# Kernel tuning notes

Hardware: AMD Instinct MI355X
Metric: run time of the kernel (lower is better)

Reference implementation:

```python
import jax, jax.numpy as jnp
import numpy as np

D_MODEL = 1024
HEADS = 16
D_K = D_MODEL // HEADS


def setup_inputs() -> dict:
    key = jax.random.key(0)
    k1, k2, k3, k4, k5 = jax.random.split(key, 5)
    B, S = 4, 2048
    q = jax.random.normal(k1, (B, S, D_MODEL), dtype=jnp.float32)
    # causal mask, broadcastable to [B, H, S, S]; 0 => masked
    mask = jnp.tril(jnp.ones((S, S), dtype=jnp.int32))[None, None, :, :]
    scale = 1.0 / np.sqrt(D_MODEL)
    w_q = jax.random.normal(k2, (D_MODEL, D_MODEL), dtype=jnp.float32) * scale
    w_k = jax.random.normal(k3, (D_MODEL, D_MODEL), dtype=jnp.float32) * scale
    w_v = jax.random.normal(k4, (D_MODEL, D_MODEL), dtype=jnp.float32) * scale
    w_o = jax.random.normal(k5, (D_MODEL, D_MODEL), dtype=jnp.float32) * scale
    return {"q": q, "mask": mask, "w_q": w_q, "w_k": w_k, "w_v": w_v, "w_o": w_o}


def reference(q, mask, w_q, w_k, w_v, w_o):
    B, S, _ = q.shape
    # Linear(bias=False): x @ W^T, then split heads -> [B, H, S, d_k]
    def proj(x, w):
        return (x @ w.T).reshape(B, S, HEADS, D_K).transpose(0, 2, 1, 3)

    Q = proj(q, w_q)
    K = proj(q, w_k)
    V = proj(q, w_v)
    scores = jnp.einsum("bhsd,bhtd->bhst", Q, K) / np.sqrt(D_K)
    scores = jnp.where(mask == 0, jnp.float32(-1e9), scores)
    attn = jax.nn.softmax(scores, axis=-1)  # dropout p=0.0 -> identity
    out = jnp.einsum("bhst,bhtd->bhsd", attn, V)
    out = out.transpose(0, 2, 1, 3).reshape(B, S, D_MODEL)
    return out @ w_o.T
```

## Files before the change

kernel.cpp:

```cpp
#include <hip/hip_runtime.h>
#include <math.h>

#define BATCH 4
#define S_LEN 2048
#define DM    1024
#define NH    16
#define DK    64

typedef __attribute__((ext_vector_type(8))) short short8;
typedef __attribute__((ext_vector_type(4))) float f32x4;

static __device__ __forceinline__ unsigned short bf_hi(float x) {
    union { float f; unsigned u; } c; c.f = x;
    return (unsigned short)(c.u >> 16);
}
static __device__ __forceinline__ float bf_f(unsigned short h) {
    union { unsigned u; float f; } c; c.u = ((unsigned)h) << 16;
    return c.f;
}
static __device__ __forceinline__ unsigned short bf_rnd(float x) {
    union { float f; unsigned u; } c; c.f = x;
    unsigned r = c.u + 0x7fffu + ((c.u >> 16) & 1u);
    return (unsigned short)(r >> 16);
}

__global__ __launch_bounds__(256, 2)
void gemm_bf16x3(const float* __restrict__ X, const float* __restrict__ W,
                 float* __restrict__ C, int M, int N, int K)
{
    __shared__ unsigned short Xh[128][40], Xl[128][40];
    __shared__ unsigned short Wh[128][40], Wl[128][40];

    const int tid  = threadIdx.x;
    const int lane = tid & 63;
    const int wid  = tid >> 6;
    const int lrow = lane & 15;
    const int lgrp = lane >> 4;
    const int bm = blockIdx.y * 128;
    const int bn = blockIdx.x * 128;
    const int wm = (wid & 1) * 64;
    const int wn = (wid >> 1) * 64;

    const f32x4 fzero = {0.f, 0.f, 0.f, 0.f};
    f32x4 acc[4][4];
#pragma unroll
    for (int i = 0; i < 4; ++i)
#pragma unroll
        for (int j = 0; j < 4; ++j) acc[i][j] = fzero;

    const int srow = tid >> 2;
    const int sc8  = (tid & 3) * 8;

    for (int kt = 0; kt < K; kt += 32) {
#pragma unroll
        for (int i = 0; i < 2; ++i) {
            const int row = srow + i * 64;
            const float* xp = X + (size_t)(bm + row) * K + kt + sc8;
            const float* wp = W + (size_t)(bn + row) * K + kt + sc8;
            float4 a0 = *(const float4*)xp, a1 = *(const float4*)(xp + 4);
            float4 b0 = *(const float4*)wp, b1 = *(const float4*)(wp + 4);
            float va[8] = {a0.x,a0.y,a0.z,a0.w,a1.x,a1.y,a1.z,a1.w};
            float vb[8] = {b0.x,b0.y,b0.z,b0.w,b1.x,b1.y,b1.z,b1.w};
            short8 xh, xl, wh, wl;
#pragma unroll
            for (int j = 0; j < 8; ++j) {
                unsigned short h = bf_hi(va[j]);
                xh[j] = (short)h; xl[j] = (short)bf_hi(va[j] - bf_f(h));
                unsigned short g = bf_hi(vb[j]);
                wh[j] = (short)g; wl[j] = (short)bf_hi(vb[j] - bf_f(g));
            }
            *(short8*)&Xh[row][sc8] = xh; *(short8*)&Xl[row][sc8] = xl;
            *(short8*)&Wh[row][sc8] = wh; *(short8*)&Wl[row][sc8] = wl;
        }
        __syncthreads();

        short8 ah[4], al[4], bh[4], bl[4];
#pragma unroll
        for (int t = 0; t < 4; ++t) {
            ah[t] = *(const short8*)&Xh[wm + t*16 + lrow][lgrp*8];
            al[t] = *(const short8*)&Xl[wm + t*16 + lrow][lgrp*8];
            bh[t] = *(const short8*)&Wh[wn + t*16 + lrow][lgrp*8];
            bl[t] = *(const short8*)&Wl[wn + t*16 + lrow][lgrp*8];
        }
#pragma unroll
        for (int mt = 0; mt < 4; ++mt)
#pragma unroll
            for (int nt = 0; nt < 4; ++nt) {
                acc[mt][nt] = __builtin_amdgcn_mfma_f32_16x16x32_bf16(ah[mt], bh[nt], acc[mt][nt], 0, 0, 0);
                acc[mt][nt] = __builtin_amdgcn_mfma_f32_16x16x32_bf16(ah[mt], bl[nt], acc[mt][nt], 0, 0, 0);
                acc[mt][nt] = __builtin_amdgcn_mfma_f32_16x16x32_bf16(al[mt], bh[nt], acc[mt][nt], 0, 0, 0);
            }
        __syncthreads();
    }

#pragma unroll
    for (int mt = 0; mt < 4; ++mt)
#pragma unroll
        for (int nt = 0; nt < 4; ++nt)
#pragma unroll
            for (int r = 0; r < 4; ++r)
                C[(size_t)(bm + wm + mt*16 + lgrp*4 + r) * N + bn + wn + nt*16 + lrow]
                    = acc[mt][nt][r];
}

__global__ __launch_bounds__(256, 2)
void attn_mfma(const float* __restrict__ Qg, const float* __restrict__ Kg,
               const float* __restrict__ Vg, float* __restrict__ Og)
{
    __shared__ unsigned short Ksh[64][72], Ksl[64][72];
    __shared__ unsigned short Vth[64][72], Vtl[64][72];
    __shared__ unsigned short Ps[4][16][72];

    const int tid  = threadIdx.x;
    const int lane = tid & 63;
    const int wid  = tid >> 6;
    const int lrow = lane & 15;
    const int lgrp = lane >> 4;

    const int rt = (int)(gridDim.x - 1u - blockIdx.x);
    const int bh = blockIdx.y;
    const int b  = bh >> 4;
    const int h  = bh & 15;

    const size_t base = (size_t)b * S_LEN * DM + (size_t)h * DK;
    const int row0 = rt * 64;

    short8 qh[2], ql[2];
#pragma unroll
    for (int c = 0; c < 2; ++c) {
        const float* qp = Qg + base + (size_t)(row0 + wid*16 + lrow) * DM + c*32 + lgrp*8;
        float4 a0 = *(const float4*)qp, a1 = *(const float4*)(qp + 4);
        float v[8] = {a0.x,a0.y,a0.z,a0.w,a1.x,a1.y,a1.z,a1.w};
#pragma unroll
        for (int j = 0; j < 8; ++j) {
            float x = v[j] * 0.125f;
            unsigned short hh = bf_hi(x);
            qh[c][j] = (short)hh;
            ql[c][j] = (short)bf_hi(x - bf_f(hh));
        }
    }

    const f32x4 fzero = {0.f, 0.f, 0.f, 0.f};
    f32x4 o[4];
    float m[4], l[4];
#pragma unroll
    for (int i = 0; i < 4; ++i) { o[i] = fzero; m[i] = -1e30f; l[i] = 0.f; }

    const int kkey = tid >> 3;
    const int kc8  = (tid & 7) * 8;
    const int vk0  = (tid >> 4) * 4;
    const int vd0  = (tid & 15) * 4;

    for (int kt = 0; kt <= rt; ++kt) {
        const float* Kb = Kg + base + (size_t)(kt * 64) * DM;
        const float* Vb = Vg + base + (size_t)(kt * 64) * DM;

#pragma unroll
        for (int i = 0; i < 2; ++i) {
            const int key = kkey + i * 32;
            const float* kp = Kb + (size_t)key * DM + kc8;
            float4 a0 = *(const float4*)kp, a1 = *(const float4*)(kp + 4);
            float v[8] = {a0.x,a0.y,a0.z,a0.w,a1.x,a1.y,a1.z,a1.w};
            short8 hh, ll;
#pragma unroll
            for (int j = 0; j < 8; ++j) {
                unsigned short t = bf_hi(v[j]);
                hh[j] = (short)t; ll[j] = (short)bf_hi(v[j] - bf_f(t));
            }
            *(short8*)&Ksh[key][kc8] = hh;
            *(short8*)&Ksl[key][kc8] = ll;
        }
        {
            float4 vv[4];
#pragma unroll
            for (int kk = 0; kk < 4; ++kk)
                vv[kk] = *(const float4*)(Vb + (size_t)(vk0 + kk) * DM + vd0);
#pragma unroll
            for (int j = 0; j < 4; ++j) {
                unsigned short h4[4], g4[4];
#pragma unroll
                for (int kk = 0; kk < 4; ++kk) {
                    float x = ((const float*)&vv[kk])[j];
                    h4[kk] = bf_hi(x);
                    g4[kk] = bf_hi(x - bf_f(h4[kk]));
                }
                uint2 wh, wl;
                wh.x = (unsigned)h4[0] | ((unsigned)h4[1] << 16);
                wh.y = (unsigned)h4[2] | ((unsigned)h4[3] << 16);
                wl.x = (unsigned)g4[0] | ((unsigned)g4[1] << 16);
                wl.y = (unsigned)g4[2] | ((unsigned)g4[3] << 16);
                *(uint2*)&Vth[vd0 + j][vk0] = wh;
                *(uint2*)&Vtl[vd0 + j][vk0] = wl;
            }
        }
        __syncthreads();

        f32x4 s[4];
#pragma unroll
        for (int t = 0; t < 4; ++t) s[t] = fzero;
#pragma unroll
        for (int t = 0; t < 4; ++t)
#pragma unroll
            for (int c = 0; c < 2; ++c) {
                short8 kh = *(const short8*)&Ksh[t*16 + lrow][c*32 + lgrp*8];
                short8 kl = *(const short8*)&Ksl[t*16 + lrow][c*32 + lgrp*8];
                s[t] = __builtin_amdgcn_mfma_f32_16x16x32_bf16(qh[c], kh, s[t], 0, 0, 0);
                s[t] = __builtin_amdgcn_mfma_f32_16x16x32_bf16(ql[c], kh, s[t], 0, 0, 0);
                s[t] = __builtin_amdgcn_mfma_f32_16x16x32_bf16(qh[c], kl, s[t], 0, 0, 0);
            }

        if (kt == rt) {
            const int qloc = wid * 16 + lgrp * 4;
#pragma unroll
            for (int t = 0; t < 4; ++t)
#pragma unroll
                for (int r = 0; r < 4; ++r)
                    if (t*16 + lrow > qloc + r) s[t][r] = -1e30f;
        }

        float pm[4];
#pragma unroll
        for (int r = 0; r < 4; ++r)
            pm[r] = fmaxf(fmaxf(s[0][r], s[1][r]), fmaxf(s[2][r], s[3][r]));
#pragma unroll
        for (int off = 8; off >= 1; off >>= 1)
#pragma unroll
            for (int r = 0; r < 4; ++r)
                pm[r] = fmaxf(pm[r], __shfl_xor(pm[r], off));

        float rs[4], rowsum[4];
#pragma unroll
        for (int r = 0; r < 4; ++r) {
            float mn = fmaxf(m[r], pm[r]);
            rs[r] = __expf(m[r] - mn);
            m[r] = mn;
            rowsum[r] = 0.f;
        }
#pragma unroll
        for (int t = 0; t < 4; ++t)
#pragma unroll
            for (int r = 0; r < 4; ++r) {
                float p = __expf(s[t][r] - m[r]);
                s[t][r] = p;
                rowsum[r] += p;
            }
#pragma unroll
        for (int off = 8; off >= 1; off >>= 1)
#pragma unroll
            for (int r = 0; r < 4; ++r)
                rowsum[r] += __shfl_xor(rowsum[r], off);
#pragma unroll
        for (int r = 0; r < 4; ++r) l[r] = l[r] * rs[r] + rowsum[r];
#pragma unroll
        for (int dt = 0; dt < 4; ++dt)
#pragma unroll
            for (int r = 0; r < 4; ++r) o[dt][r] *= rs[r];

#pragma unroll
        for (int t = 0; t < 4; ++t)
#pragma unroll
            for (int r = 0; r < 4; ++r)
                Ps[wid][lgrp*4 + r][t*16 + lrow] = bf_rnd(s[t][r]);

#pragma unroll
        for (int kc = 0; kc < 2; ++kc) {
            short8 pa = *(const short8*)&Ps[wid][lrow][kc*32 + lgrp*8];
#pragma unroll
            for (int dt = 0; dt < 4; ++dt) {
                short8 vh = *(const short8*)&Vth[dt*16 + lrow][kc*32 + lgrp*8];
                short8 vl = *(const short8*)&Vtl[dt*16 + lrow][kc*32 + lgrp*8];
                o[dt] = __builtin_amdgcn_mfma_f32_16x16x32_bf16(pa, vh, o[dt], 0, 0, 0);
                o[dt] = __builtin_amdgcn_mfma_f32_16x16x32_bf16(pa, vl, o[dt], 0, 0, 0);
            }
        }
        __syncthreads();
    }

    float* Ob = Og + base;
#pragma unroll
    for (int r = 0; r < 4; ++r) {
        float inv = 1.f / l[r];
#pragma unroll
        for (int dt = 0; dt < 4; ++dt)
            Ob[(size_t)(row0 + wid*16 + lgrp*4 + r) * DM + dt*16 + lrow] = o[dt][r] * inv;
    }
}

extern "C" void kernel_launch(void* const* d_in, const int* in_sizes, int n_in,
                              void* d_out, int out_size, void* d_ws, size_t ws_size,
                              hipStream_t stream)
{
    const float* q   = (const float*)d_in[0];
    const float* w_q = (const float*)d_in[2];
    const float* w_k = (const float*)d_in[3];
    const float* w_v = (const float*)d_in[4];
    const float* w_o = (const float*)d_in[5];
    float* out = (float*)d_out;

    const size_t MN = (size_t)BATCH * S_LEN * DM;
    float* Qw = (float*)d_ws;
    float* Kw = Qw + MN;
    float* Vw = Kw + MN;
    float* Ow = Qw;

    const int M = BATCH * S_LEN;
    dim3 blk(256);
    dim3 ggrid(DM / 128, M / 128);
    gemm_bf16x3<<<ggrid, blk, 0, stream>>>(q, w_q, Qw, M, DM, DM);
    gemm_bf16x3<<<ggrid, blk, 0, stream>>>(q, w_k, Kw, M, DM, DM);
    gemm_bf16x3<<<ggrid, blk, 0, stream>>>(q, w_v, Vw, M, DM, DM);

    dim3 agrid(S_LEN / 64, BATCH * NH);
    attn_mfma<<<agrid, blk, 0, stream>>>(Qw, Kw, Vw, Ow);

    gemm_bf16x3<<<ggrid, blk, 0, stream>>>(Ow, w_o, out, M, DM, DM);
}
```

Before: 880.5 us.

## Store Q/K/V/O as pre-split bf16 hi/lo pairs instead of fp32

The projection GEMMs now emit bf16 hi/lo split outputs, with the 1/sqrt(d_k) scale folded into the Q projection. The attention kernel reads these directly instead of re-splitting fp32 K/V on every key tile, and the output GEMM consumes the pre-split O. Traffic per element is the same, but the repeated per-tile split arithmetic in attention goes away. Launch bounds are also raised to 3 blocks per SM to lift occupancy, at the risk of register spills.

```diff
diff --git a/kernel.cpp b/kernel.cpp
--- a/kernel.cpp
+++ b/kernel.cpp
@@ -24,9 +24,16 @@
     return (unsigned short)(r >> 16);
 }
 
-__global__ __launch_bounds__(256, 2)
-void gemm_bf16x3(const float* __restrict__ X, const float* __restrict__ W,
-                 float* __restrict__ C, int M, int N, int K)
+template<bool PRESPLIT_A, bool SPLIT_OUT>
+__global__ __launch_bounds__(256, 3)
+void gemm_k(const float* __restrict__ Af,
+            const unsigned short* __restrict__ Agh,
+            const unsigned short* __restrict__ Agl,
+            const float* __restrict__ W,
+            float* __restrict__ Cf,
+            unsigned short* __restrict__ Ch,
+            unsigned short* __restrict__ Cl,
+            float scale, int M, int N, int K)
 {
     __shared__ unsigned short Xh[128][40], Xl[128][40];
     __shared__ unsigned short Wh[128][40], Wl[128][40];
@@ -52,24 +59,45 @@
     const int sc8  = (tid & 3) * 8;
 
     for (int kt = 0; kt < K; kt += 32) {
+        if constexpr (PRESPLIT_A) {
+#pragma unroll
+            for (int p = 0; p < 2; ++p) {
+                int pos = tid + p * 256;
+                int row = pos >> 2;
+                int c8  = (pos & 3) * 8;
+                *(short8*)&Xh[row][c8] =
+                    *(const short8*)(Agh + (size_t)(bm + row) * K + kt + c8);
+                *(short8*)&Xl[row][c8] =
+                    *(const short8*)(Agl + (size_t)(bm + row) * K + kt + c8);
+            }
+        } else {
+#pragma unroll
+            for (int i = 0; i < 2; ++i) {
+                const int row = srow + i * 64;
+                const float* xp = Af + (size_t)(bm + row) * K + kt + sc8;
+                float4 a0 = *(const float4*)xp, a1 = *(const float4*)(xp + 4);
+                float va[8] = {a0.x,a0.y,a0.z,a0.w,a1.x,a1.y,a1.z,a1.w};
+                short8 xh, xl;
+#pragma unroll
+                for (int j = 0; j < 8; ++j) {
+                    unsigned short h = bf_hi(va[j]);
+                    xh[j] = (short)h; xl[j] = (short)bf_hi(va[j] - bf_f(h));
+                }
+                *(short8*)&Xh[row][sc8] = xh; *(short8*)&Xl[row][sc8] = xl;
+            }
+        }
 #pragma unroll
         for (int i = 0; i < 2; ++i) {
             const int row = srow + i * 64;
-            const float* xp = X + (size_t)(bm + row) * K + kt + sc8;
             const float* wp = W + (size_t)(bn + row) * K + kt + sc8;
-            float4 a0 = *(const float4*)xp, a1 = *(const float4*)(xp + 4);
             float4 b0 = *(const float4*)wp, b1 = *(const float4*)(wp + 4);
-            float va[8] = {a0.x,a0.y,a0.z,a0.w,a1.x,a1.y,a1.z,a1.w};
             float vb[8] = {b0.x,b0.y,b0.z,b0.w,b1.x,b1.y,b1.z,b1.w};
-            short8 xh, xl, wh, wl;
+            short8 wh, wl;
 #pragma unroll
             for (int j = 0; j < 8; ++j) {
-                unsigned short h = bf_hi(va[j]);
-                xh[j] = (short)h; xl[j] = (short)bf_hi(va[j] - bf_f(h));
                 unsigned short g = bf_hi(vb[j]);
                 wh[j] = (short)g; wl[j] = (short)bf_hi(vb[j] - bf_f(g));
             }
-            *(short8*)&Xh[row][sc8] = xh; *(short8*)&Xl[row][sc8] = xl;
             *(short8*)&Wh[row][sc8] = wh; *(short8*)&Wl[row][sc8] = wl;
         }
         __syncthreads();
@@ -98,14 +126,25 @@
 #pragma unroll
         for (int nt = 0; nt < 4; ++nt)
 #pragma unroll
-            for (int r = 0; r < 4; ++r)
-                C[(size_t)(bm + wm + mt*16 + lgrp*4 + r) * N + bn + wn + nt*16 + lrow]
-                    = acc[mt][nt][r];
-}
-
-__global__ __launch_bounds__(256, 2)
-void attn_mfma(const float* __restrict__ Qg, const float* __restrict__ Kg,
-               const float* __restrict__ Vg, float* __restrict__ Og)
+            for (int r = 0; r < 4; ++r) {
+                const size_t idx = (size_t)(bm + wm + mt*16 + lgrp*4 + r) * N
+                                 + bn + wn + nt*16 + lrow;
+                if constexpr (SPLIT_OUT) {
+                    float v = acc[mt][nt][r] * scale;
+                    unsigned short h = bf_hi(v);
+                    Ch[idx] = h;
+                    Cl[idx] = bf_hi(v - bf_f(h));
+                } else {
+                    Cf[idx] = acc[mt][nt][r];
+                }
+            }
+}
+
+__global__ __launch_bounds__(256, 3)
+void attn_mfma(const unsigned short* __restrict__ Qh_g, const unsigned short* __restrict__ Ql_g,
+               const unsigned short* __restrict__ Kh_g, const unsigned short* __restrict__ Kl_g,
+               const unsigned short* __restrict__ Vh_g, const unsigned short* __restrict__ Vl_g,
+               unsigned short* __restrict__ Oh_g, unsigned short* __restrict__ Ol_g)
 {
     __shared__ unsigned short Ksh[64][72], Ksl[64][72];
     __shared__ unsigned short Vth[64][72], Vtl[64][72];
@@ -128,16 +167,9 @@
     short8 qh[2], ql[2];
 #pragma unroll
     for (int c = 0; c < 2; ++c) {
-        const float* qp = Qg + base + (size_t)(row0 + wid*16 + lrow) * DM + c*32 + lgrp*8;
-        float4 a0 = *(const float4*)qp, a1 = *(const float4*)(qp + 4);
-        float v[8] = {a0.x,a0.y,a0.z,a0.w,a1.x,a1.y,a1.z,a1.w};
-#pragma unroll
-        for (int j = 0; j < 8; ++j) {
-            float x = v[j] * 0.125f;
-            unsigned short hh = bf_hi(x);
-            qh[c][j] = (short)hh;
-            ql[c][j] = (short)bf_hi(x - bf_f(hh));
-        }
+        const size_t qoff = base + (size_t)(row0 + wid*16 + lrow) * DM + c*32 + lgrp*8;
+        qh[c] = *(const short8*)(Qh_g + qoff);
+        ql[c] = *(const short8*)(Ql_g + qoff);
     }
 
     const f32x4 fzero = {0.f, 0.f, 0.f, 0.f};
@@ -146,49 +178,44 @@
 #pragma unroll
     for (int i = 0; i < 4; ++i) { o[i] = fzero; m[i] = -1e30f; l[i] = 0.f; }
 
-    const int kkey = tid >> 3;
-    const int kc8  = (tid & 7) * 8;
+    const int skey = tid >> 3;
+    const int sc8  = (tid & 7) * 8;
     const int vk0  = (tid >> 4) * 4;
     const int vd0  = (tid & 15) * 4;
 
     for (int kt = 0; kt <= rt; ++kt) {
-        const float* Kb = Kg + base + (size_t)(kt * 64) * DM;
-        const float* Vb = Vg + base + (size_t)(kt * 64) * DM;
+        const size_t kb = base + (size_t)(kt * 64) * DM;
 
 #pragma unroll
         for (int i = 0; i < 2; ++i) {
-            const int key = kkey + i * 32;
-            const float* kp = Kb + (size_t)key * DM + kc8;
-            float4 a0 = *(const float4*)kp, a1 = *(const float4*)(kp + 4);
-            float v[8] = {a0.x,a0.y,a0.z,a0.w,a1.x,a1.y,a1.z,a1.w};
-            short8 hh, ll;
-#pragma unroll
-            for (int j = 0; j < 8; ++j) {
-                unsigned short t = bf_hi(v[j]);
-                hh[j] = (short)t; ll[j] = (short)bf_hi(v[j] - bf_f(t));
-            }
-            *(short8*)&Ksh[key][kc8] = hh;
-            *(short8*)&Ksl[key][kc8] = ll;
+            const int key = skey + i * 32;
+            const size_t off = kb + (size_t)key * DM + sc8;
+            *(short8*)&Ksh[key][sc8] = *(const short8*)(Kh_g + off);
+            *(short8*)&Ksl[key][sc8] = *(const short8*)(Kl_g + off);
         }
         {
-            float4 vv[4];
-#pragma unroll
-            for (int kk = 0; kk < 4; ++kk)
-                vv[kk] = *(const float4*)(Vb + (size_t)(vk0 + kk) * DM + vd0);
+            ushort4 ah4[4], al4[4];
+#pragma unroll
+            for (int kk = 0; kk < 4; ++kk) {
+                const size_t off = kb + (size_t)(vk0 + kk) * DM + vd0;
+                ah4[kk] = *(const ushort4*)(Vh_g + off);
+                al4[kk] = *(const ushort4*)(Vl_g + off);
+            }
 #pragma unroll
             for (int j = 0; j < 4; ++j) {
-                unsigned short h4[4], g4[4];
-#pragma unroll
-                for (int kk = 0; kk < 4; ++kk) {
-                    float x = ((const float*)&vv[kk])[j];
-                    h4[kk] = bf_hi(x);
-                    g4[kk] = bf_hi(x - bf_f(h4[kk]));
-                }
+                const unsigned short* e0 = (const unsigned short*)&ah4[0];
+                const unsigned short* e1 = (const unsigned short*)&ah4[1];
+                const unsigned short* e2 = (const unsigned short*)&ah4[2];
+                const unsigned short* e3 = (const unsigned short*)&ah4[3];
                 uint2 wh, wl;
-                wh.x = (unsigned)h4[0] | ((unsigned)h4[1] << 16);
-                wh.y = (unsigned)h4[2] | ((unsigned)h4[3] << 16);
-                wl.x = (unsigned)g4[0] | ((unsigned)g4[1] << 16);
-                wl.y = (unsigned)g4[2] | ((unsigned)g4[3] << 16);
+                wh.x = (unsigned)e0[j] | ((unsigned)e1[j] << 16);
+                wh.y = (unsigned)e2[j] | ((unsigned)e3[j] << 16);
+                const unsigned short* f0 = (const unsigned short*)&al4[0];
+                const unsigned short* f1 = (const unsigned short*)&al4[1];
+                const unsigned short* f2 = (const unsigned short*)&al4[2];
+                const unsigned short* f3 = (const unsigned short*)&al4[3];
+                wl.x = (unsigned)f0[j] | ((unsigned)f1[j] << 16);
+                wl.y = (unsigned)f2[j] | ((unsigned)f3[j] << 16);
                 *(uint2*)&Vth[vd0 + j][vk0] = wh;
                 *(uint2*)&Vtl[vd0 + j][vk0] = wl;
             }
@@ -276,13 +303,17 @@
         __syncthreads();
     }
 
-    float* Ob = Og + base;
 #pragma unroll
     for (int r = 0; r < 4; ++r) {
         float inv = 1.f / l[r];
 #pragma unroll
-        for (int dt = 0; dt < 4; ++dt)
-            Ob[(size_t)(row0 + wid*16 + lgrp*4 + r) * DM + dt*16 + lrow] = o[dt][r] * inv;
+        for (int dt = 0; dt < 4; ++dt) {
+            const size_t idx = base + (size_t)(row0 + wid*16 + lgrp*4 + r) * DM + dt*16 + lrow;
+            float v = o[dt][r] * inv;
+            unsigned short hh = bf_hi(v);
+            Oh_g[idx] = hh;
+            Ol_g[idx] = bf_hi(v - bf_f(hh));
+        }
     }
 }
 
@@ -297,21 +328,29 @@
     const float* w_o = (const float*)d_in[5];
     float* out = (float*)d_out;
 
-    const size_t MN = (size_t)BATCH * S_LEN * DM;
-    float* Qw = (float*)d_ws;
-    float* Kw = Qw + MN;
-    float* Vw = Kw + MN;
-    float* Ow = Qw;
+    const size_t HN = (size_t)BATCH * S_LEN * DM;
+    unsigned short* Qh = (unsigned short*)d_ws;
+    unsigned short* Ql = Qh + HN;
+    unsigned short* Kh = Ql + HN;
+    unsigned short* Kl = Kh + HN;
+    unsigned short* Vh = Kl + HN;
+    unsigned short* Vl = Vh + HN;
+    unsigned short* Oh = Qh;
+    unsigned short* Ol = Ql;
 
     const int M = BATCH * S_LEN;
     dim3 blk(256);
     dim3 ggrid(DM / 128, M / 128);
-    gemm_bf16x3<<<ggrid, blk, 0, stream>>>(q, w_q, Qw, M, DM, DM);
-    gemm_bf16x3<<<ggrid, blk, 0, stream>>>(q, w_k, Kw, M, DM, DM);
-    gemm_bf16x3<<<ggrid, blk, 0, stream>>>(q, w_v, Vw, M, DM, DM);
+    gemm_k<false, true><<<ggrid, blk, 0, stream>>>(q, nullptr, nullptr, w_q,
+                                                   nullptr, Qh, Ql, 0.125f, M, DM, DM);
+    gemm_k<false, true><<<ggrid, blk, 0, stream>>>(q, nullptr, nullptr, w_k,
+                                                   nullptr, Kh, Kl, 1.0f, M, DM, DM);
+    gemm_k<false, true><<<ggrid, blk, 0, stream>>>(q, nullptr, nullptr, w_v,
+                                                   nullptr, Vh, Vl, 1.0f, M, DM, DM);
 
     dim3 agrid(S_LEN / 64, BATCH * NH);
-    attn_mfma<<<agrid, blk, 0, stream>>>(Qw, Kw, Vw, Ow);
-
-    gemm_bf16x3<<<ggrid, blk, 0, stream>>>(Ow, w_o, out, M, DM, DM);
-}
+    attn_mfma<<<agrid, blk, 0, stream>>>(Qh, Ql, Kh, Kl, Vh, Vl, Oh, Ol);
+
+    gemm_k<true, false><<<ggrid, blk, 0, stream>>>(nullptr, Oh, Ol, w_o,
+                                                   out, nullptr, nullptr, 1.0f, M, DM, DM);
+}
```

Result: faster. 756.6 us (-14.1%).
